# Optimization experiments

Measured on AMD Instinct MI355X. Metric: run time of the kernel, lower is better.

The kernel has to match this reference:

```python
import jax, jax.numpy as jnp
import numpy as np

EMBED_DIM = 1536
BOTTLENECK = 64
EPS = 1e-5  # torch LayerNorm default


def setup_inputs() -> dict:
    key = jax.random.key(0)
    ks = jax.random.split(key, 6)
    x = jax.random.normal(ks[0], (32768, EMBED_DIM), dtype=jnp.float32)
    # Xavier-uniform init for down (matches nn.init.xavier_uniform_)
    limit = float(np.sqrt(6.0 / (EMBED_DIM + BOTTLENECK)))
    w_down = jax.random.uniform(ks[1], (BOTTLENECK, EMBED_DIM), jnp.float32, -limit, limit)
    b_down = jnp.zeros((BOTTLENECK,), jnp.float32)
    # Torch initializes up to zeros; use small random values so gradients/outputs are non-trivial
    w_up = jax.random.normal(ks[2], (EMBED_DIM, BOTTLENECK), dtype=jnp.float32) * 0.02
    b_up = jnp.zeros((EMBED_DIM,), jnp.float32)
    gamma = jnp.ones((EMBED_DIM,), jnp.float32)
    beta = jnp.zeros((EMBED_DIM,), jnp.float32)
    return {"x": x, "w_down": w_down, "b_down": b_down, "w_up": w_up,
            "b_up": b_up, "gamma": gamma, "beta": beta}


def reference(x, w_down, b_down, w_up, b_up, gamma, beta):
    residual = x
    # LayerNorm over last dim
    mean = jnp.mean(x, axis=-1, keepdims=True)
    var = jnp.mean(jnp.square(x - mean), axis=-1, keepdims=True)
    h = (x - mean) * jax.lax.rsqrt(var + EPS) * gamma + beta
    # down-proj -> exact GELU -> (dropout=identity at inference) -> up-proj
    h = jnp.einsum('nd,bd->nb', h, w_down) + b_down  # [N, 64]
    h = jax.nn.gelu(h, approximate=False)            # torch F.gelu default (erf)
    h = jnp.einsum('nb,db->nd', h, w_up) + b_up      # [N, 1536]
    out = residual + h
    # F.normalize(p=2, dim=-1) with eps=1e-12
    norm = jnp.maximum(jnp.linalg.norm(out, axis=-1, keepdims=True), 1e-12)
    return out / norm
```

## Files before the change

### kernel.cpp

```cpp
#include <hip/hip_runtime.h>
#include <math.h>

#define EMBED 1536
#define BN 64
#define XS_STRIDE 1544
#define GS_STRIDE 80

typedef __attribute__((ext_vector_type(8))) short short8;
typedef __attribute__((ext_vector_type(4))) float f32x4;

__device__ inline unsigned short f2bf(float f) {
    union { float f; unsigned u; } c; c.f = f;
    unsigned u = c.u;
    return (unsigned short)((u + 0x7fffu + ((u >> 16) & 1u)) >> 16);
}

__global__ void conv_kernel(const float* __restrict__ w_down, const float* __restrict__ w_up,
                            unsigned short* __restrict__ wdb, unsigned short* __restrict__ wub) {
    int i = blockIdx.x * blockDim.x + threadIdx.x;
    if (i < BN * EMBED) {
        wdb[i] = f2bf(w_down[i]);
        wub[i] = f2bf(w_up[i]);
    }
}

__global__ void c12_kernel(const float* __restrict__ w_down, const float* __restrict__ gamma,
                           const float* __restrict__ beta, float* __restrict__ c1,
                           float* __restrict__ c2) {
    int b = blockIdx.x;
    int t = threadIdx.x;
    float s1 = 0.f, s2 = 0.f;
    for (int d = t; d < EMBED; d += 256) {
        float w = w_down[b * EMBED + d];
        s1 += gamma[d] * w;
        s2 += beta[d] * w;
    }
    #pragma unroll
    for (int m = 1; m < 64; m <<= 1) { s1 += __shfl_xor(s1, m); s2 += __shfl_xor(s2, m); }
    __shared__ float r1[4], r2[4];
    int wave = t >> 6, lane = t & 63;
    if (lane == 0) { r1[wave] = s1; r2[wave] = s2; }
    __syncthreads();
    if (t == 0) {
        c1[b] = r1[0] + r1[1] + r1[2] + r1[3];
        c2[b] = r2[0] + r2[1] + r2[2] + r2[3];
    }
}

__global__ __launch_bounds__(256) void fused_kernel(
    const float* __restrict__ x, const float* __restrict__ b_down,
    const float* __restrict__ b_up, const float* __restrict__ gamma,
    const unsigned short* __restrict__ wdb, const unsigned short* __restrict__ wub,
    const float* __restrict__ c1, const float* __restrict__ c2,
    float* __restrict__ out)
{
    __shared__ unsigned short xs[16 * XS_STRIDE];
    __shared__ unsigned short gs[16 * GS_STRIDE];
    __shared__ float mean_s[16], rstd_s[16], sumsq_s[16], inv_s[16];

    const int tid  = threadIdx.x;
    const int wave = tid >> 6, lane = tid & 63;
    const int l16  = lane & 15, quad = lane >> 4;
    const long row0 = (long)blockIdx.x * 16;

    const float4* gp = (const float4*)gamma;
    #pragma unroll
    for (int j = 0; j < 4; ++j) {
        int lr = wave * 4 + j;
        const float4* xp = (const float4*)(x + (row0 + lr) * EMBED);
        float4 v[6];
        float s = 0.f, ss = 0.f;
        #pragma unroll
        for (int k = 0; k < 6; ++k) {
            v[k] = xp[lane + 64 * k];
            s  += v[k].x + v[k].y + v[k].z + v[k].w;
            ss += v[k].x * v[k].x + v[k].y * v[k].y + v[k].z * v[k].z + v[k].w * v[k].w;
        }
        #pragma unroll
        for (int m = 1; m < 64; m <<= 1) { s += __shfl_xor(s, m); ss += __shfl_xor(ss, m); }
        float mean = s * (1.f / EMBED);
        float var  = ss * (1.f / EMBED) - mean * mean;
        float rstd = rsqrtf(var + 1e-5f);
        if (lane == 0) { mean_s[lr] = mean; rstd_s[lr] = rstd; sumsq_s[lr] = 0.f; }
        #pragma unroll
        for (int k = 0; k < 6; ++k) {
            float4 g4 = gp[lane + 64 * k];
            ushort4 p;
            p.x = f2bf(v[k].x * g4.x); p.y = f2bf(v[k].y * g4.y);
            p.z = f2bf(v[k].z * g4.z); p.w = f2bf(v[k].w * g4.w);
            *(ushort4*)(&xs[lr * XS_STRIDE + 4 * (lane + 64 * k)]) = p;
        }
    }
    __syncthreads();

    f32x4 acc = {0.f, 0.f, 0.f, 0.f};
    {
        const unsigned short* arow = &xs[l16 * XS_STRIDE];
        const unsigned short* brow = wdb + (size_t)(wave * 16 + l16) * EMBED;
        #pragma unroll 4
        for (int kk = 0; kk < 48; ++kk) {
            int ko = kk * 32 + quad * 8;
            short8 a = *(const short8*)(arow + ko);
            short8 b = *(const short8*)(brow + ko);
            acc = __builtin_amdgcn_mfma_f32_16x16x32_bf16(a, b, acc, 0, 0, 0);
        }
    }
    {
        int bg = wave * 16 + l16;
        float c1v = c1[bg], c2v = c2[bg], bdv = b_down[bg];
        #pragma unroll
        for (int reg = 0; reg < 4; ++reg) {
            int r = quad * 4 + reg;
            float rs = rstd_s[r];
            float v = rs * acc[reg] - rs * mean_s[r] * c1v + c2v + bdv;
            float g = 0.5f * v * (1.f + erff(v * 0.70710678118654752f));
            gs[r * GS_STRIDE + bg] = f2bf(g);
        }
    }
    __syncthreads();

    short8 a0 = *(const short8*)(&gs[l16 * GS_STRIDE + quad * 8]);
    short8 a1 = *(const short8*)(&gs[l16 * GS_STRIDE + 32 + quad * 8]);
    float sq[4] = {0.f, 0.f, 0.f, 0.f};

    for (int pass = 0; pass < 2; ++pass) {
        #pragma unroll 2
        for (int t = 0; t < 24; ++t) {
            int d = wave * 384 + t * 16 + l16;
            float bu = b_up[d];
            f32x4 c;
            #pragma unroll
            for (int reg = 0; reg < 4; ++reg)
                c[reg] = x[(row0 + quad * 4 + reg) * EMBED + d] + bu;
            const unsigned short* wrow = wub + (size_t)d * 64;
            short8 b0 = *(const short8*)(wrow + quad * 8);
            short8 b1 = *(const short8*)(wrow + 32 + quad * 8);
            c = __builtin_amdgcn_mfma_f32_16x16x32_bf16(a0, b0, c, 0, 0, 0);
            c = __builtin_amdgcn_mfma_f32_16x16x32_bf16(a1, b1, c, 0, 0, 0);
            if (pass == 0) {
                #pragma unroll
                for (int reg = 0; reg < 4; ++reg) sq[reg] += c[reg] * c[reg];
            } else {
                #pragma unroll
                for (int reg = 0; reg < 4; ++reg)
                    out[(row0 + quad * 4 + reg) * EMBED + d] = c[reg] * inv_s[quad * 4 + reg];
            }
        }
        if (pass == 0) {
            #pragma unroll
            for (int m = 1; m < 16; m <<= 1) {
                #pragma unroll
                for (int reg = 0; reg < 4; ++reg) sq[reg] += __shfl_xor(sq[reg], m);
            }
            if (l16 == 0) {
                #pragma unroll
                for (int reg = 0; reg < 4; ++reg) atomicAdd(&sumsq_s[quad * 4 + reg], sq[reg]);
            }
            __syncthreads();
            if (tid < 16) inv_s[tid] = 1.f / fmaxf(sqrtf(sumsq_s[tid]), 1e-12f);
            __syncthreads();
        }
    }
}

extern "C" void kernel_launch(void* const* d_in, const int* in_sizes, int n_in,
                              void* d_out, int out_size, void* d_ws, size_t ws_size,
                              hipStream_t stream)
{
    const float* x      = (const float*)d_in[0];
    const float* w_down = (const float*)d_in[1];
    const float* b_down = (const float*)d_in[2];
    const float* w_up   = (const float*)d_in[3];
    const float* b_up   = (const float*)d_in[4];
    const float* gamma  = (const float*)d_in[5];
    const float* beta   = (const float*)d_in[6];
    float* out = (float*)d_out;

    const int N = in_sizes[0] / EMBED;

    unsigned short* wdb = (unsigned short*)d_ws;
    unsigned short* wub = wdb + BN * EMBED;
    float* c1 = (float*)(wub + BN * EMBED);
    float* c2 = c1 + BN;

    conv_kernel<<<(BN * EMBED + 255) / 256, 256, 0, stream>>>(w_down, w_up, wdb, wub);
    c12_kernel<<<BN, 256, 0, stream>>>(w_down, gamma, beta, c1, c2);
    fused_kernel<<<N / 16, 256, 0, stream>>>(x, b_down, b_up, gamma, wdb, wub, c1, c2, out);
}
```

Before: 490.6 us.

## Single-pass up-projection with register-held outputs and residual from LDS bf16 copy

Holds the up-projection results in registers so the L2-normalisation needs only one pass, and takes the residual from the bf16 x tile already in shared memory instead of reloading x from global twice. The MFMA operands are swapped so each lane writes contiguous float4 outputs. Gamma is folded into the down-projection weights, and the two prep kernels are merged into one launch. The residual now carries bf16 rounding, which reduces accuracy, and the 24 accumulators raise register pressure.

```diff
diff --git a/kernel.cpp b/kernel.cpp
--- a/kernel.cpp
+++ b/kernel.cpp
@@ -14,20 +14,24 @@
     unsigned u = c.u;
     return (unsigned short)((u + 0x7fffu + ((u >> 16) & 1u)) >> 16);
 }
-
-__global__ void conv_kernel(const float* __restrict__ w_down, const float* __restrict__ w_up,
-                            unsigned short* __restrict__ wdb, unsigned short* __restrict__ wub) {
-    int i = blockIdx.x * blockDim.x + threadIdx.x;
-    if (i < BN * EMBED) {
-        wdb[i] = f2bf(w_down[i]);
-        wub[i] = f2bf(w_up[i]);
-    }
+__device__ inline float bf2f(unsigned short h) {
+    union { unsigned u; float f; } c; c.u = ((unsigned)h) << 16;
+    return c.f;
 }
 
-__global__ void c12_kernel(const float* __restrict__ w_down, const float* __restrict__ gamma,
-                           const float* __restrict__ beta, float* __restrict__ c1,
-                           float* __restrict__ c2) {
-    int b = blockIdx.x;
+__global__ void prep_kernel(const float* __restrict__ w_down, const float* __restrict__ w_up,
+                            const float* __restrict__ gamma, const float* __restrict__ beta,
+                            unsigned short* __restrict__ wdg, unsigned short* __restrict__ wub,
+                            float* __restrict__ c1, float* __restrict__ c2) {
+    int blk = blockIdx.x;
+    if (blk < 384) {
+        int i = blk * 256 + threadIdx.x;
+        int d = i % EMBED;
+        wdg[i] = f2bf(w_down[i] * gamma[d]);
+        wub[i] = f2bf(w_up[i]);
+        return;
+    }
+    int b = blk - 384;
     int t = threadIdx.x;
     float s1 = 0.f, s2 = 0.f;
     for (int d = t; d < EMBED; d += 256) {
@@ -47,10 +51,10 @@
     }
 }
 
-__global__ __launch_bounds__(256) void fused_kernel(
+__global__ __launch_bounds__(256, 3) void fused_kernel(
     const float* __restrict__ x, const float* __restrict__ b_down,
-    const float* __restrict__ b_up, const float* __restrict__ gamma,
-    const unsigned short* __restrict__ wdb, const unsigned short* __restrict__ wub,
+    const float* __restrict__ b_up,
+    const unsigned short* __restrict__ wdg, const unsigned short* __restrict__ wub,
     const float* __restrict__ c1, const float* __restrict__ c2,
     float* __restrict__ out)
 {
@@ -63,32 +67,40 @@
     const int l16  = lane & 15, quad = lane >> 4;
     const long row0 = (long)blockIdx.x * 16;
 
-    const float4* gp = (const float4*)gamma;
-    #pragma unroll
-    for (int j = 0; j < 4; ++j) {
-        int lr = wave * 4 + j;
-        const float4* xp = (const float4*)(x + (row0 + lr) * EMBED);
-        float4 v[6];
-        float s = 0.f, ss = 0.f;
+    {
+        float4 v[4][6];
         #pragma unroll
-        for (int k = 0; k < 6; ++k) {
-            v[k] = xp[lane + 64 * k];
-            s  += v[k].x + v[k].y + v[k].z + v[k].w;
-            ss += v[k].x * v[k].x + v[k].y * v[k].y + v[k].z * v[k].z + v[k].w * v[k].w;
+        for (int j = 0; j < 4; ++j) {
+            const float4* xp = (const float4*)(x + (row0 + wave * 4 + j) * EMBED);
+            #pragma unroll
+            for (int k = 0; k < 6; ++k) v[j][k] = xp[lane + 64 * k];
         }
         #pragma unroll
-        for (int m = 1; m < 64; m <<= 1) { s += __shfl_xor(s, m); ss += __shfl_xor(ss, m); }
-        float mean = s * (1.f / EMBED);
-        float var  = ss * (1.f / EMBED) - mean * mean;
-        float rstd = rsqrtf(var + 1e-5f);
-        if (lane == 0) { mean_s[lr] = mean; rstd_s[lr] = rstd; sumsq_s[lr] = 0.f; }
-        #pragma unroll
-        for (int k = 0; k < 6; ++k) {
-            float4 g4 = gp[lane + 64 * k];
-            ushort4 p;
-            p.x = f2bf(v[k].x * g4.x); p.y = f2bf(v[k].y * g4.y);
-            p.z = f2bf(v[k].z * g4.z); p.w = f2bf(v[k].w * g4.w);
-            *(ushort4*)(&xs[lr * XS_STRIDE + 4 * (lane + 64 * k)]) = p;
+        for (int j = 0; j < 4; ++j) {
+            int lr = wave * 4 + j;
+            float s = 0.f, ss = 0.f;
+            #pragma unroll
+            for (int k = 0; k < 6; ++k) {
+                s  += v[j][k].x + v[j][k].y + v[j][k].z + v[j][k].w;
+                ss += v[j][k].x * v[j][k].x + v[j][k].y * v[j][k].y
+                    + v[j][k].z * v[j][k].z + v[j][k].w * v[j][k].w;
+            }
+            #pragma unroll
+            for (int m = 1; m < 64; m <<= 1) { s += __shfl_xor(s, m); ss += __shfl_xor(ss, m); }
+            float mean = s * (1.f / EMBED);
+            float var  = ss * (1.f / EMBED) - mean * mean;
+            if (lane == 0) {
+                mean_s[lr] = mean;
+                rstd_s[lr] = rsqrtf(var + 1e-5f);
+                sumsq_s[lr] = 0.f;
+            }
+            #pragma unroll
+            for (int k = 0; k < 6; ++k) {
+                ushort4 p;
+                p.x = f2bf(v[j][k].x); p.y = f2bf(v[j][k].y);
+                p.z = f2bf(v[j][k].z); p.w = f2bf(v[j][k].w);
+                *(ushort4*)(&xs[lr * XS_STRIDE + 4 * (lane + 64 * k)]) = p;
+            }
         }
     }
     __syncthreads();
@@ -96,7 +108,7 @@
     f32x4 acc = {0.f, 0.f, 0.f, 0.f};
     {
         const unsigned short* arow = &xs[l16 * XS_STRIDE];
-        const unsigned short* brow = wdb + (size_t)(wave * 16 + l16) * EMBED;
+        const unsigned short* brow = wdg + (size_t)(wave * 16 + l16) * EMBED;
         #pragma unroll 4
         for (int kk = 0; kk < 48; ++kk) {
             int ko = kk * 32 + quad * 8;
@@ -119,47 +131,46 @@
     }
     __syncthreads();
 
-    short8 a0 = *(const short8*)(&gs[l16 * GS_STRIDE + quad * 8]);
-    short8 a1 = *(const short8*)(&gs[l16 * GS_STRIDE + 32 + quad * 8]);
-    float sq[4] = {0.f, 0.f, 0.f, 0.f};
+    short8 gb0 = *(const short8*)(&gs[l16 * GS_STRIDE + quad * 8]);
+    short8 gb1 = *(const short8*)(&gs[l16 * GS_STRIDE + 32 + quad * 8]);
+    const int dbase = wave * 384;
+    f32x4 cc[24];
+    float sqs = 0.f;
+    #pragma unroll
+    for (int t = 0; t < 24; ++t) {
+        int d0 = dbase + t * 16;
+        int dm = d0 + quad * 4;
+        float4 bu = *(const float4*)(b_up + dm);
+        ushort4 rx = *(const ushort4*)(&xs[l16 * XS_STRIDE + dm]);
+        f32x4 c;
+        c[0] = bf2f(rx.x) + bu.x;
+        c[1] = bf2f(rx.y) + bu.y;
+        c[2] = bf2f(rx.z) + bu.z;
+        c[3] = bf2f(rx.w) + bu.w;
+        const unsigned short* wrow = wub + (size_t)(d0 + l16) * 64;
+        short8 a0 = *(const short8*)(wrow + quad * 8);
+        short8 a1 = *(const short8*)(wrow + 32 + quad * 8);
+        c = __builtin_amdgcn_mfma_f32_16x16x32_bf16(a0, gb0, c, 0, 0, 0);
+        c = __builtin_amdgcn_mfma_f32_16x16x32_bf16(a1, gb1, c, 0, 0, 0);
+        cc[t] = c;
+        sqs += c[0] * c[0] + c[1] * c[1] + c[2] * c[2] + c[3] * c[3];
+    }
+    sqs += __shfl_xor(sqs, 16);
+    sqs += __shfl_xor(sqs, 32);
+    if (lane < 16) atomicAdd(&sumsq_s[l16], sqs);
+    __syncthreads();
+    if (tid < 16) inv_s[tid] = 1.f / fmaxf(sqrtf(sumsq_s[tid]), 1e-12f);
+    __syncthreads();
 
-    for (int pass = 0; pass < 2; ++pass) {
-        #pragma unroll 2
-        for (int t = 0; t < 24; ++t) {
-            int d = wave * 384 + t * 16 + l16;
-            float bu = b_up[d];
-            f32x4 c;
-            #pragma unroll
-            for (int reg = 0; reg < 4; ++reg)
-                c[reg] = x[(row0 + quad * 4 + reg) * EMBED + d] + bu;
-            const unsigned short* wrow = wub + (size_t)d * 64;
-            short8 b0 = *(const short8*)(wrow + quad * 8);
-            short8 b1 = *(const short8*)(wrow + 32 + quad * 8);
-            c = __builtin_amdgcn_mfma_f32_16x16x32_bf16(a0, b0, c, 0, 0, 0);
-            c = __builtin_amdgcn_mfma_f32_16x16x32_bf16(a1, b1, c, 0, 0, 0);
-            if (pass == 0) {
-                #pragma unroll
-                for (int reg = 0; reg < 4; ++reg) sq[reg] += c[reg] * c[reg];
-            } else {
-                #pragma unroll
-                for (int reg = 0; reg < 4; ++reg)
-                    out[(row0 + quad * 4 + reg) * EMBED + d] = c[reg] * inv_s[quad * 4 + reg];
-            }
-        }
-        if (pass == 0) {
-            #pragma unroll
-            for (int m = 1; m < 16; m <<= 1) {
-                #pragma unroll
-                for (int reg = 0; reg < 4; ++reg) sq[reg] += __shfl_xor(sq[reg], m);
-            }
-            if (l16 == 0) {
-                #pragma unroll
-                for (int reg = 0; reg < 4; ++reg) atomicAdd(&sumsq_s[quad * 4 + reg], sq[reg]);
-            }
-            __syncthreads();
-            if (tid < 16) inv_s[tid] = 1.f / fmaxf(sqrtf(sumsq_s[tid]), 1e-12f);
-            __syncthreads();
-        }
+    const float inv = inv_s[l16];
+    float* orow = out + (row0 + l16) * EMBED;
+    #pragma unroll
+    for (int t = 0; t < 24; ++t) {
+        int dm = dbase + t * 16 + quad * 4;
+        f32x4 c = cc[t];
+        float4 o;
+        o.x = c[0] * inv; o.y = c[1] * inv; o.z = c[2] * inv; o.w = c[3] * inv;
+        *(float4*)(orow + dm) = o;
     }
 }
 
@@ -178,12 +189,11 @@
 
     const int N = in_sizes[0] / EMBED;
 
-    unsigned short* wdb = (unsigned short*)d_ws;
-    unsigned short* wub = wdb + BN * EMBED;
+    unsigned short* wdg = (unsigned short*)d_ws;
+    unsigned short* wub = wdg + BN * EMBED;
     float* c1 = (float*)(wub + BN * EMBED);
     float* c2 = c1 + BN;
 
-    conv_kernel<<<(BN * EMBED + 255) / 256, 256, 0, stream>>>(w_down, w_up, wdb, wub);
-    c12_kernel<<<BN, 256, 0, stream>>>(w_down, gamma, beta, c1, c2);
-    fused_kernel<<<N / 16, 256, 0, stream>>>(x, b_down, b_up, gamma, wdb, wub, c1, c2, out);
+    prep_kernel<<<384 + BN, 256, 0, stream>>>(w_down, w_up, gamma, beta, wdg, wub, c1, c2);
+    fused_kernel<<<N / 16, 256, 0, stream>>>(x, b_down, b_up, wdg, wub, c1, c2, out);
 }
```

After: 415.4 us. 15.3% less time.
